# Performance work log

Measured on AMD Instinct MI355X. Metric: run time of the kernel, lower is better.

Reference implementation:

```python
import jax, jax.numpy as jnp
import numpy as np

D_MODEL = 192; D_STATE = 16; EXPAND = 2; D_INNER = EXPAND * D_MODEL
DT_RANK = 12  # ceil(192/16)
SG_HID = 6 * D_STATE  # SimpleGate1D expansion_factor=6
B, H, W = 4, 64, 64

def setup_inputs() -> dict:
    key = jax.random.key(0)
    ks = jax.random.split(key, 24)
    f = lambda i, shape, s=0.02: jax.random.normal(ks[i], shape, jnp.float32) * s
    # dt bias init per SS2D.dt_init: inverse-softplus of dt ~ logU(1e-3, 1e-1)
    dt = jnp.exp(jax.random.uniform(ks[20], (D_INNER,)) * (np.log(0.1) - np.log(0.001)) + np.log(0.001))
    dt = jnp.maximum(dt, 1e-4)
    inv_dt = dt + jnp.log(-jnp.expm1(-dt))
    return {
        "x": jax.random.normal(ks[0], (B, H, W, D_MODEL), jnp.float32),
        "low": jax.random.normal(ks[1], (B, H, W, D_MODEL), jnp.float32),
        "ln_g": jnp.ones((D_MODEL,), jnp.float32), "ln_b": jnp.zeros((D_MODEL,), jnp.float32),
        "in_proj_w": f(2, (2 * D_INNER, D_MODEL)),
        "in_proj_low_w": f(3, (D_INNER, D_MODEL)),
        "conv2d_w": f(4, (D_INNER, 1, 3, 3), 0.1), "conv2d_b": jnp.zeros((D_INNER,), jnp.float32),
        "x_proj_w": f(5, (DT_RANK + 2 * D_STATE, D_INNER)),
        "x_proj_w_low": f(6, (DT_RANK + 2 * D_STATE, D_INNER)),
        "conv_dt_w": f(7, (DT_RANK, 1, 15), 0.05),
        "conv_B_w": f(8, (D_STATE, 1, 15), 0.05),
        "conv_C_w": f(9, (D_STATE, 1, 15), 0.05),
        "sgb_w1": f(10, (2 * SG_HID, D_STATE), 0.1), "sgb_w2": f(11, (D_STATE, SG_HID), 0.1),
        "sgc_w1": f(12, (2 * SG_HID, D_STATE), 0.1), "sgc_w2": f(13, (D_STATE, SG_HID), 0.1),
        "dt_projs_w": f(14, (D_INNER, DT_RANK), 0.2), "dt_projs_b": inv_dt,
        "A_logs": jnp.tile(jnp.log(jnp.arange(1, D_STATE + 1, dtype=jnp.float32))[None, :], (D_INNER, 1)),
        "Ds": jnp.ones((D_INNER,), jnp.float32),
        "out_norm_g": jnp.ones((D_INNER,), jnp.float32), "out_norm_b": jnp.zeros((D_INNER,), jnp.float32),
        "out_proj_w": f(15, (D_MODEL, D_INNER)),
    }

def _ln(x, g, b):
    m = x.mean(-1, keepdims=True)
    v = x.var(-1, keepdims=True)
    return (x - m) * jax.lax.rsqrt(v + 1e-5) * g + b

def _dwconv1d(x, w, dil=2):  # x [B,C,L], w [C,1,K], depthwise, length-preserving
    pad = dil * (w.shape[-1] - 1) // 2
    return jax.lax.conv_general_dilated(x, w, (1,), [(pad, pad)], rhs_dilation=(dil,),
                                        dimension_numbers=('NCH', 'OIH', 'NCH'),
                                        feature_group_count=x.shape[1])

def _sgate(x, w1, w2):  # SimpleGate1D on [B,C,L]: fc1 -> gelu(x1)*x2 -> fc2 along C
    y = jnp.einsum('bcl,hc->bhl', x, w1)
    hid = w2.shape[1]
    g = jax.nn.gelu(y[:, :hid], approximate=False) * y[:, hid:]
    return jnp.einsum('bhl,ch->bcl', g, w2)

def _selective_scan(u, delta, A, Bs, Cs, D):
    # u,delta:[B,Di,L] A:[Di,N] Bs,Cs:[B,N,L] D:[Di]  (Mamba S6 recurrence)
    def step(h, t):
        d_t, u_t, B_t, C_t = t  # [B,Di],[B,Di],[B,N],[B,N]
        h = jnp.exp(d_t[..., None] * A) * h + (d_t * u_t)[..., None] * B_t[:, None, :]
        return h, jnp.einsum('bdn,bn->bd', h, C_t)
    h0 = jnp.zeros((u.shape[0], u.shape[1], A.shape[1]), u.dtype)
    xs = (jnp.moveaxis(delta, -1, 0), jnp.moveaxis(u, -1, 0),
          jnp.moveaxis(Bs, -1, 0), jnp.moveaxis(Cs, -1, 0))
    _, ys = jax.lax.scan(step, h0, xs)  # ys [L,B,Di]
    return jnp.moveaxis(ys, 0, -1) + u * D[:, None]

def reference(x, low, ln_g, ln_b, in_proj_w, in_proj_low_w, conv2d_w, conv2d_b,
              x_proj_w, x_proj_w_low, conv_dt_w, conv_B_w, conv_C_w,
              sgb_w1, sgb_w2, sgc_w1, sgc_w2, dt_projs_w, dt_projs_b,
              A_logs, Ds, out_norm_g, out_norm_b, out_proj_w):
    Bb, Hh, Ww, C = x.shape
    L = Hh * Ww
    R = conv_dt_w.shape[0]
    N = A_logs.shape[1]
    xn = _ln(x, ln_g, ln_b)                       # VSSBlock pre-LN
    xz = xn @ in_proj_w.T                         # [B,H,W,2*Di]
    xh, z = jnp.split(xz, 2, axis=-1)
    lowp = (low @ in_proj_low_w.T).transpose(0, 3, 1, 2)  # [B,Di,H,W]
    xc = xh.transpose(0, 3, 1, 2)
    xc = jax.lax.conv_general_dilated(xc, conv2d_w, (1, 1), [(1, 1), (1, 1)],
                                      dimension_numbers=('NCHW', 'OIHW', 'NCHW'),
                                      feature_group_count=xc.shape[1]) + conv2d_b[None, :, None, None]
    xc = jax.nn.silu(xc)
    xs = xc.reshape(Bb, -1, L)
    lows = lowp.reshape(Bb, -1, L)
    # low-branch projections (dt, B, C) with SimpleGate on B/C
    low_dbl = jnp.einsum('bdl,cd->bcl', lows, x_proj_w_low)
    dts_l, Bs_l, Cs_l = jnp.split(low_dbl, [R, R + N], axis=1)
    Bs_l = _sgate(Bs_l, sgb_w1, sgb_w2)
    Cs_l = _sgate(Cs_l, sgc_w1, sgc_w2)
    # high-branch projections
    x_dbl = jnp.einsum('bdl,cd->bcl', xs, x_proj_w)
    dts, Bs, Cs = jnp.split(x_dbl, [R, R + N], axis=1)
    dts = dts + dts_l; Bs = Bs + Bs_l; Cs = Cs + Cs_l
    # residual dilated depthwise 1D refinement of dt/B/C along L
    dts = dts + _dwconv1d(dts, conv_dt_w)
    Bs = Bs + _dwconv1d(Bs, conv_B_w)
    Cs = Cs + _dwconv1d(Cs, conv_C_w)
    delta = jax.nn.softplus(jnp.einsum('brl,dr->bdl', dts, dt_projs_w) + dt_projs_b[None, :, None])
    y = _selective_scan(xs, delta, -jnp.exp(A_logs), Bs, Cs, Ds)   # [B,Di,L]
    y = _ln(y.reshape(Bb, -1, Hh, Ww).transpose(0, 2, 3, 1), out_norm_g, out_norm_b)
    y = y * jax.nn.silu(z)
    return x + y @ out_proj_w.T  # VSSBlock residual
```

## Files before the change

kernel.cpp:

```cpp
#include <hip/hip_runtime.h>
#include <math.h>

#define LL 4096
#define NBATCH 4
#define CM 192
#define DI 384
#define NST 16
#define RK 12
#define NCH 44
#define SGH 96

typedef unsigned short ushort_t;
typedef __attribute__((ext_vector_type(8))) short bf16x8;
typedef __attribute__((ext_vector_type(4))) float f32x4;
typedef __attribute__((ext_vector_type(8))) unsigned short ushort8;
typedef __attribute__((ext_vector_type(4))) unsigned short ushort4v;

#define O_WT_IN   0
#define O_WT_LOW  147456
#define O_WT_XP   221184
#define O_WT_XPL  245760
#define O_WT_OUT  270336
#define O_XN      344064
#define O_LOWT    3489792
#define O_XH      6635520
#define O_Z       12926976
#define O_LOWP    19218432
#define O_XS      25509888
#define O_DBCH    31801344
#define O_DBCL    32522240
#define O_DBC     33243136
#define O_BS      33964032
#define O_CS      34226176
#define O_DELTA   O_LOWP
#define O_Y       O_XH
#define O_Y1      O_XN
#define O_DTS     O_DBCH

__device__ __forceinline__ ushort_t f2bf(float v) {
    unsigned u = __float_as_uint(v);
    return (ushort_t)((u + 0x7FFFu + ((u >> 16) & 1u)) >> 16);
}
__device__ __forceinline__ float bf2f(ushort_t h) {
    return __uint_as_float(((unsigned)h) << 16);
}

__device__ __forceinline__ int permidx(int l) {
    return ((l >> 2) & 3) * 1024 + ((l >> 4) << 2) + (l & 3);
}

#define LD16P(dst, row, t4) { \
  float4 _a = *(const float4*)((row) + (t4)); \
  float4 _b = *(const float4*)((row) + 1024 + (t4)); \
  float4 _c = *(const float4*)((row) + 2048 + (t4)); \
  float4 _d = *(const float4*)((row) + 3072 + (t4)); \
  dst[0]=_a.x; dst[1]=_a.y; dst[2]=_a.z; dst[3]=_a.w; \
  dst[4]=_b.x; dst[5]=_b.y; dst[6]=_b.z; dst[7]=_b.w; \
  dst[8]=_c.x; dst[9]=_c.y; dst[10]=_c.z; dst[11]=_c.w; \
  dst[12]=_d.x; dst[13]=_d.y; dst[14]=_d.z; dst[15]=_d.w; }

__global__ __launch_bounds__(256) void prep_kernel(
    const float* __restrict__ i0, ushort_t* h0, ushort_t* l0_,
    const float* __restrict__ i1, ushort_t* h1, ushort_t* l1,
    const float* __restrict__ i2, ushort_t* h2, ushort_t* l2,
    const float* __restrict__ p0, ushort_t* ph0, ushort_t* pl0,
    const float* __restrict__ p1, ushort_t* ph1, ushort_t* pl1,
    const float* __restrict__ X, const float* __restrict__ gw, const float* __restrict__ bw,
    ushort_t* __restrict__ oh, ushort_t* __restrict__ ol,
    const float* __restrict__ LOW, ushort_t* __restrict__ lh, ushort_t* __restrict__ llo)
{
    __shared__ float xt[64][193];
    __shared__ float reds[64][4], redq[64][4];
    __shared__ float mu_s[64], rs_s[64];
    int bx = blockIdx.x;
    int tid = threadIdx.x;
    if (bx < 288) {
        const float* in; ushort_t* oh_; ushort_t* ol_; int base;
        if (bx < 144)      { in = i0; oh_ = h0; ol_ = l0_; base = bx * 1024; }
        else if (bx < 216) { in = i1; oh_ = h1; ol_ = l1;  base = (bx-144) * 1024; }
        else               { in = i2; oh_ = h2; ol_ = l2;  base = (bx-216) * 1024; }
        int i = base + tid * 4;
        float4 v = *(const float4*)&in[i];
        ushort4v h, l;
        h.x = f2bf(v.x); l.x = f2bf(v.x - bf2f(h.x));
        h.y = f2bf(v.y); l.y = f2bf(v.y - bf2f(h.y));
        h.z = f2bf(v.z); l.z = f2bf(v.z - bf2f(h.z));
        h.w = f2bf(v.w); l.w = f2bf(v.w - bf2f(h.w));
        *(ushort4v*)&oh_[i] = h;
        *(ushort4v*)&ol_[i] = l;
        return;
    }
    if (bx < 336) {
        int bb = bx - 288;
        int sel = bb / 24, bxx = bb % 24;
        const float* in = sel ? p1 : p0;
        ushort_t* oh_ = sel ? ph1 : ph0;
        ushort_t* ol_ = sel ? pl1 : pl0;
        int idx = (bxx * 256 + tid) * 4;
        int n = idx / 384;
        float4 v = (n < NCH) ? *(const float4*)&in[idx] : make_float4(0.f,0.f,0.f,0.f);
        ushort4v h, l;
        h.x = f2bf(v.x); l.x = f2bf(v.x - bf2f(h.x));
        h.y = f2bf(v.y); l.y = f2bf(v.y - bf2f(h.y));
        h.z = f2bf(v.z); l.z = f2bf(v.z - bf2f(h.z));
        h.w = f2bf(v.w); l.w = f2bf(v.w - bf2f(h.w));
        *(ushort4v*)&oh_[idx] = h;
        *(ushort4v*)&ol_[idx] = l;
        return;
    }
    int ax = bx - 336;
    if (ax >= 256) {
        int i = ((ax - 256) * 256 + tid) * 4;
        float4 v = *(const float4*)&LOW[i];
        ushort4v h, l;
        h.x = f2bf(v.x); l.x = f2bf(v.x - bf2f(h.x));
        h.y = f2bf(v.y); l.y = f2bf(v.y - bf2f(h.y));
        h.z = f2bf(v.z); l.z = f2bf(v.z - bf2f(h.z));
        h.w = f2bf(v.w); l.w = f2bf(v.w - bf2f(h.w));
        *(ushort4v*)&lh[i] = h;
        *(ushort4v*)&llo[i] = l;
        return;
    }
    int t0 = ax * 64;
    const float* Xb = X + (size_t)t0 * CM;
#pragma unroll
    for (int i = 0; i < 12; i++) {
        int f4 = tid + 256 * i;
        float4 v = *(const float4*)&Xb[f4 * 4];
        int row = f4 / 48, c = (f4 % 48) * 4;
        xt[row][c] = v.x; xt[row][c+1] = v.y; xt[row][c+2] = v.z; xt[row][c+3] = v.w;
    }
    __syncthreads();
    int tok = tid & 63, p = tid >> 6;
    float s = 0.f, q = 0.f;
#pragma unroll 8
    for (int i = 0; i < 48; i++) { float v = xt[tok][p*48+i]; s += v; q = fmaf(v, v, q); }
    reds[tok][p] = s; redq[tok][p] = q;
    __syncthreads();
    if (tid < 64) {
        float ss = reds[tid][0]+reds[tid][1]+reds[tid][2]+reds[tid][3];
        float qq = redq[tid][0]+redq[tid][1]+redq[tid][2]+redq[tid][3];
        float mu = ss * (1.f/CM);
        float var = qq * (1.f/CM) - mu*mu;
        mu_s[tid] = mu; rs_s[tid] = rsqrtf(var + 1e-5f);
    }
    __syncthreads();
    int tok2 = tid >> 2, c0 = (tid & 3) * 48;
    float mu = mu_s[tok2], rs = rs_s[tok2];
    size_t tb = (size_t)(t0 + tok2) * CM;
#pragma unroll 8
    for (int i = 0; i < 48; i++) {
        int c = c0 + i;
        float v = (xt[tok2][c] - mu) * rs * gw[c] + bw[c];
        ushort_t h = f2bf(v);
        oh[tb + c] = h;
        ol[tb + c] = f2bf(v - bf2f(h));
    }
}

__global__ __launch_bounds__(256) void gemm_inlow(
    const ushort_t* __restrict__ xnh, const ushort_t* __restrict__ xnl,
    const ushort_t* __restrict__ wInH, const ushort_t* __restrict__ wInL,
    const ushort_t* __restrict__ lowh, const ushort_t* __restrict__ lowl,
    const ushort_t* __restrict__ wLowH, const ushort_t* __restrict__ wLowL,
    float* __restrict__ xh, float* __restrict__ z, float* __restrict__ lowp)
{
    __shared__ __align__(16) char smem[32768];
    ushort_t* sAh = (ushort_t*)smem;
    ushort_t* sAl = sAh + 4096;
    ushort_t* sWh = sAh + 8192;
    ushort_t* sWl = sAh + 12288;
    const int KDIM = 192;
    int tid = threadIdx.x;
    int t0 = blockIdx.x * 128;
    int b = t0 >> 12, l0 = t0 & 4095;
    int ysel = blockIdx.y;
    bool isLow = ysel >= 6;
    int n0 = (isLow ? (ysel - 6) : ysel) * 128;
    const ushort_t* Ahi = isLow ? lowh : xnh;
    const ushort_t* Alo = isLow ? lowl : xnl;
    const ushort_t* Whi = isLow ? wLowH : wInH;
    const ushort_t* Wlo = isLow ? wLowL : wInL;
    int arow = tid >> 1, kgA = (tid & 1) * 2;
    const ushort_t* gAh = Ahi + (size_t)(t0 + arow) * KDIM + kgA * 8;
    const ushort_t* gAl = Alo + (size_t)(t0 + arow) * KDIM + kgA * 8;
    const ushort_t* gWh = Whi + (size_t)(n0 + arow) * KDIM + kgA * 8;
    const ushort_t* gWl = Wlo + (size_t)(n0 + arow) * KDIM + kgA * 8;
    int lane = tid & 63, w = tid >> 6;
    int ln = lane & 15, kg = lane >> 4;
    int am0 = w * 32 + ln;
    f32x4 acc[2][8];
#pragma unroll
    for (int mf = 0; mf < 2; mf++)
#pragma unroll
        for (int nf = 0; nf < 8; nf++) acc[mf][nf] = (f32x4){0.f, 0.f, 0.f, 0.f};

    for (int k0 = 0; k0 < KDIM; k0 += 32) {
        __syncthreads();
        {
            ushort8 a0 = *(const ushort8*)(gAh + k0);
            ushort8 a1 = *(const ushort8*)(gAh + k0 + 8);
            *(ushort8*)(sAh + kgA*1024 + arow*8) = a0;
            *(ushort8*)(sAh + (kgA+1)*1024 + arow*8) = a1;
            ushort8 b0 = *(const ushort8*)(gAl + k0);
            ushort8 b1 = *(const ushort8*)(gAl + k0 + 8);
            *(ushort8*)(sAl + kgA*1024 + arow*8) = b0;
            *(ushort8*)(sAl + (kgA+1)*1024 + arow*8) = b1;
            ushort8 w0 = *(const ushort8*)(gWh + k0);
            ushort8 w1 = *(const ushort8*)(gWh + k0 + 8);
            *(ushort8*)(sWh + kgA*1024 + arow*8) = w0;
            *(ushort8*)(sWh + (kgA+1)*1024 + arow*8) = w1;
            ushort8 w2 = *(const ushort8*)(gWl + k0);
            ushort8 w3 = *(const ushort8*)(gWl + k0 + 8);
            *(ushort8*)(sWl + kgA*1024 + arow*8) = w2;
            *(ushort8*)(sWl + (kgA+1)*1024 + arow*8) = w3;
        }
        __syncthreads();
        bf16x8 aH[2], aL[2];
#pragma unroll
        for (int mf = 0; mf < 2; mf++) {
            aH[mf] = *(const bf16x8*)(sAh + kg*1024 + (am0 + mf*16)*8);
            aL[mf] = *(const bf16x8*)(sAl + kg*1024 + (am0 + mf*16)*8);
        }
#pragma unroll
        for (int half = 0; half < 2; half++) {
            bf16x8 bH[4], bL[4];
#pragma unroll
            for (int n4 = 0; n4 < 4; n4++) {
                int nr = (half*4 + n4)*16 + ln;
                bH[n4] = *(const bf16x8*)(sWh + kg*1024 + nr*8);
                bL[n4] = *(const bf16x8*)(sWl + kg*1024 + nr*8);
            }
#pragma unroll
            for (int mf = 0; mf < 2; mf++)
#pragma unroll
                for (int n4 = 0; n4 < 4; n4++) {
                    int nf = half*4 + n4;
                    acc[mf][nf] = __builtin_amdgcn_mfma_f32_16x16x32_bf16(aH[mf], bH[n4], acc[mf][nf], 0, 0, 0);
                    acc[mf][nf] = __builtin_amdgcn_mfma_f32_16x16x32_bf16(aH[mf], bL[n4], acc[mf][nf], 0, 0, 0);
                    acc[mf][nf] = __builtin_amdgcn_mfma_f32_16x16x32_bf16(aL[mf], bH[n4], acc[mf][nf], 0, 0, 0);
                }
        }
    }
#pragma unroll
    for (int mf = 0; mf < 2; mf++) {
        int l = l0 + w*32 + mf*16 + kg*4;
#pragma unroll
        for (int nf = 0; nf < 8; nf++) {
            int n = n0 + nf*16 + ln;
            float* dst;
            if (!isLow) {
                dst = (n < DI) ? (xh + ((size_t)b*DI + n)*LL + l)
                               : (z  + ((size_t)b*DI + (n - DI))*LL + l);
            } else {
                dst = lowp + ((size_t)b*DI + n)*LL + l;
            }
            *(f32x4*)dst = acc[mf][nf];
        }
    }
}

template<int MODE, int SPLIT, int PERM0>
__global__ __launch_bounds__(256) void gemm_cmaj(
    const float* __restrict__ A0, const float* __restrict__ A1,
    const ushort_t* __restrict__ W0h, const ushort_t* __restrict__ W0l,
    const ushort_t* __restrict__ W1h, const ushort_t* __restrict__ W1l,
    const float* __restrict__ resid,
    float* __restrict__ o0, float* __restrict__ o1, int Nreal)
{
    __shared__ __align__(16) float sA[32*68];
    __shared__ __align__(16) ushort_t sWh[4*64*8];
    __shared__ __align__(16) ushort_t sWl[4*64*8];
    bool sel = (blockIdx.z == 1);
    const float* A = sel ? A1 : A0;
    const ushort_t* Wh = sel ? W1h : W0h;
    const ushort_t* Wl = sel ? W1l : W0l;
    float* out0 = sel ? o1 : o0;
    const bool perm = sel ? false : (PERM0 != 0);
    int tid = threadIdx.x;
    int t0 = blockIdx.x * 64;
    int b = t0 >> 12, l0 = t0 & 4095;
    int n0 = blockIdx.y * 64;
    const float* Ab = A + (size_t)b * 384 * LL;
    int wrow = tid >> 2, kgW = tid & 3;
    int lane = tid & 63, w = tid >> 6;
    int ln = lane & 15, kg = lane >> 4;
    int am0 = w * 16 + ln;
    f32x4 acc[4];
#pragma unroll
    for (int nf = 0; nf < 4; nf++) acc[nf] = (f32x4){0.f, 0.f, 0.f, 0.f};

    for (int k0 = 0; k0 < 384; k0 += 32) {
        __syncthreads();
#pragma unroll
        for (int i = 0; i < 2; i++) {
            int idx = tid + 256*i;
            int row = idx >> 4, ch = idx & 15;
            int m = ch * 4;
            int src = perm ? (((m >> 2) & 3) * 1024 + (((l0 + m) >> 4) << 2))
                           : (l0 + m);
            float4 v = *(const float4*)&Ab[(size_t)(k0 + row)*LL + src];
            *(float4*)&sA[row*68 + m] = v;
        }
        {
            ushort8 wv = *(const ushort8*)(Wh + (size_t)(n0 + wrow)*384 + k0 + kgW*8);
            *(ushort8*)(sWh + kgW*512 + wrow*8) = wv;
            if (SPLIT == 3) {
                ushort8 wl = *(const ushort8*)(Wl + (size_t)(n0 + wrow)*384 + k0 + kgW*8);
                *(ushort8*)(sWl + kgW*512 + wrow*8) = wl;
            }
        }
        __syncthreads();
        bf16x8 aH, aL;
#pragma unroll
        for (int e = 0; e < 8; e++) {
            float v = sA[(kg*8 + e)*68 + am0];
            ushort_t h = f2bf(v);
            aH[e] = (short)h;
            if (SPLIT == 3) aL[e] = (short)f2bf(v - bf2f(h));
        }
        bf16x8 bH[4], bL[4];
#pragma unroll
        for (int nf = 0; nf < 4; nf++) {
            bH[nf] = *(const bf16x8*)(sWh + kg*512 + (nf*16 + ln)*8);
            if (SPLIT == 3) bL[nf] = *(const bf16x8*)(sWl + kg*512 + (nf*16 + ln)*8);
        }
#pragma unroll
        for (int nf = 0; nf < 4; nf++) {
            acc[nf] = __builtin_amdgcn_mfma_f32_16x16x32_bf16(aH, bH[nf], acc[nf], 0, 0, 0);
            if (SPLIT == 3) {
                acc[nf] = __builtin_amdgcn_mfma_f32_16x16x32_bf16(aH, bL[nf], acc[nf], 0, 0, 0);
                acc[nf] = __builtin_amdgcn_mfma_f32_16x16x32_bf16(aL, bH[nf], acc[nf], 0, 0, 0);
            }
        }
    }

    if (MODE == 2) {
#pragma unroll
        for (int j = 0; j < 4; j++) {
            int t = t0 + w*16 + kg*4 + j;
#pragma unroll
            for (int nf = 0; nf < 4; nf++) {
                int n = n0 + nf*16 + ln;
                out0[(size_t)t*CM + n] = resid[(size_t)t*CM + n] + acc[nf][j];
            }
        }
    } else {
        int l = l0 + w*16 + kg*4;
#pragma unroll
        for (int nf = 0; nf < 4; nf++) {
            int n = n0 + nf*16 + ln;
            if (n < Nreal)
                *(f32x4*)(out0 + ((size_t)b*Nreal + n)*LL + l) = acc[nf];
        }
    }
}

__global__ __launch_bounds__(256) void conv2d_silu_kernel(const float* __restrict__ xh,
    const float* __restrict__ w, const float* __restrict__ bias, float* __restrict__ xs)
{
    int tid = threadIdx.x;
    int l = blockIdx.x * 256 + tid;
    int c = blockIdx.y, b = blockIdx.z;
    const float* P = xh + ((size_t)b*DI + c)*LL;
    int h = l >> 6, ww = l & 63;
    float acc = bias[c];
#pragma unroll
    for (int kh = 0; kh < 3; kh++) {
        int hh = h + kh - 1;
        if ((unsigned)hh < 64u) {
#pragma unroll
            for (int kw = 0; kw < 3; kw++) {
                int wv = ww + kw - 1;
                if ((unsigned)wv < 64u) acc = fmaf(w[c*9 + kh*3 + kw], P[hh*64 + wv], acc);
            }
        }
    }
    float sg = 1.f / (1.f + __expf(-acc));
    xs[((size_t)b*DI + c)*LL + permidx(l)] = acc * sg;
}

__global__ __launch_bounds__(256) void gates_kernel(const float* __restrict__ dbcH,
    const float* __restrict__ dbcL,
    const float* __restrict__ sgb1, const float* __restrict__ sgb2,
    const float* __restrict__ sgc1, const float* __restrict__ sgc2,
    float* __restrict__ dbc)
{
    __shared__ float w1[192*16];
    __shared__ float w2[16*96];
    __shared__ float red[4][16][64];
    int tid = threadIdx.x;
    int gate = blockIdx.z;
    const float* g1 = gate ? sgc1 : sgb1;
    const float* g2 = gate ? sgc2 : sgb2;
    for (int i = tid; i < 192*16; i += 256) w1[i] = g1[i];
    for (int i = tid; i < 16*96;  i += 256) w2[i] = g2[i];
    int lq = tid & 63, p = tid >> 6;
    int l = blockIdx.x * 64 + lq;
    int b = blockIdx.y;
    size_t pb_ = (size_t)b*NCH*LL + l;
    __syncthreads();
    if (!gate) {
#pragma unroll
        for (int i = 0; i < 3; i++) {
            int c = p*3 + i;
            dbc[pb_ + (size_t)c*LL] = dbcH[pb_ + (size_t)c*LL] + dbcL[pb_ + (size_t)c*LL];
        }
    }
    int coff = RK + gate*NST;
    float xin[16], og[16];
#pragma unroll
    for (int n = 0; n < 16; n++) { xin[n] = dbcL[pb_ + (size_t)(coff+n)*LL]; og[n] = 0.f; }
    int h0 = p * 24;
    for (int h = h0; h < h0 + 24; h++) {
        float ya = 0.f, yb = 0.f;
#pragma unroll
        for (int n = 0; n < 16; n++) {
            ya = fmaf(w1[h*16+n], xin[n], ya);
            yb = fmaf(w1[(h+SGH)*16+n], xin[n], yb);
        }
        float gg = 0.5f * ya * (1.f + erff(ya * 0.70710678f)) * yb;
#pragma unroll
        for (int n = 0; n < 16; n++) og[n] = fmaf(w2[n*SGH+h], gg, og[n]);
    }
#pragma unroll
    for (int n = 0; n < 16; n++) red[p][n][lq] = og[n];
    __syncthreads();
#pragma unroll
    for (int i = 0; i < 4; i++) {
        int n = p*4 + i;
        float v = red[0][n][lq] + red[1][n][lq] + red[2][n][lq] + red[3][n][lq];
        dbc[pb_ + (size_t)(coff+n)*LL] = dbcH[pb_ + (size_t)(coff+n)*LL] + v;
    }
}

__global__ __launch_bounds__(256) void conv_dbc_kernel(const float* __restrict__ dbc,
    const float* __restrict__ wdt, const float* __restrict__ wB, const float* __restrict__ wC,
    float* __restrict__ dts, float* __restrict__ Bs, float* __restrict__ Cs)
{
    int l = blockIdx.x * 256 + threadIdx.x;
    int c = blockIdx.y, b = blockIdx.z;
    const float* wsrc = (c < RK) ? (wdt + c*15)
                      : (c < RK+NST ? wB + (c-RK)*15 : wC + (c-RK-NST)*15);
    float w[15];
#pragma unroll
    for (int k = 0; k < 15; k++) w[k] = wsrc[k];
    const float* P = dbc + ((size_t)b*NCH + c)*LL;
    float a = P[l];
#pragma unroll
    for (int k = 0; k < 15; k++) {
        int lt = l + 2*k - 14;
        if ((unsigned)lt < (unsigned)LL) a = fmaf(w[k], P[lt], a);
    }
    if (c < RK)            dts[((size_t)b*RK  + c)*LL + l] = a;
    else if (c < RK+NST)   Bs [((size_t)b*NST + (c-RK))*LL + permidx(l)] = a;
    else                   Cs [((size_t)b*NST + (c-RK-NST))*LL + permidx(l)] = a;
}

__global__ __launch_bounds__(256) void delta_kernel(const float* __restrict__ dts,
    const float* __restrict__ dtw, const float* __restrict__ dtb, float* __restrict__ delta)
{
    __shared__ float sdt[RK][128];
    __shared__ float sw[64][RK];
    int tid = threadIdx.x;
    int l0 = blockIdx.x * 128, d0 = blockIdx.y * 64, b = blockIdx.z;
    for (int i = tid; i < RK*128; i += 256) {
        int r = i >> 7, lq = i & 127;
        sdt[r][lq] = dts[((size_t)b*RK + r)*LL + l0 + lq];
    }
    for (int i = tid; i < 64*RK; i += 256) {
        int dq = i / RK, r = i - dq*RK;
        sw[dq][r] = dtw[(size_t)(d0+dq)*RK + r];
    }
    __syncthreads();
    int lq = tid & 63, g = tid >> 6;
    for (int dd = 0; dd < 16; dd++) {
        int dqq = g*16 + dd, d = d0 + dqq;
        float wr[RK];
#pragma unroll
        for (int r = 0; r < RK; r++) wr[r] = sw[dqq][r];
        float bias = dtb[d];
#pragma unroll
        for (int li = 0; li < 2; li++) {
            int lloc = lq + li*64;
            float s = bias;
#pragma unroll
            for (int r = 0; r < RK; r++) s = fmaf(wr[r], sdt[r][lloc], s);
            float sp = fmaxf(s, 0.f) + __logf(1.f + __expf(-fabsf(s)));
            delta[((size_t)b*DI + d)*LL + permidx(l0 + lloc)] = sp;
        }
    }
}

__global__ __launch_bounds__(256) void scan_kernel(
    const float* __restrict__ u_, const float* __restrict__ delta_,
    const float* __restrict__ Bs_, const float* __restrict__ Cs_,
    const float* __restrict__ Alogs, const float* __restrict__ Ds,
    float* __restrict__ y0_, float* __restrict__ y1_)
{
    __shared__ float wAs[8][4], wBs[8][4];
    __shared__ float yt[16][258];
    int tid = threadIdx.x;
    int t4 = tid * 4;
    int bid = blockIdx.x;
    int half = bid & 1, bd = bid >> 1;
    int b = bd / DI, d = bd % DI;
    int n0 = half * 8;
    size_t rowoff = ((size_t)b*DI + d)*LL;
    float dl[16], du[16], yac[16];
    LD16P(du, u_ + rowoff, t4);
    LD16P(dl, delta_ + rowoff, t4);
    float Dd = Ds[d];
#pragma unroll
    for (int s = 0; s < 16; s++) {
        yac[s] = half ? 0.f : du[s]*Dd;
        du[s] = dl[s]*du[s];
    }
    int lane = tid & 63, w = tid >> 6;
#pragma unroll 1
    for (int j = 0; j < 8; j++) {
        float An = -__expf(Alogs[d*NST + n0 + j]);
        float Bn[16], Cn[16], t[16];
        LD16P(Bn, Bs_ + ((size_t)b*NST + n0 + j)*LL, t4);
        LD16P(Cn, Cs_ + ((size_t)b*NST + n0 + j)*LL, t4);
        float a = 1.f, h = 0.f;
#pragma unroll
        for (int s = 0; s < 16; s++) {
            float e = __expf(dl[s]*An);
            a *= e;
            h = fmaf(e, h, du[s]*Bn[s]);
            yac[s] = fmaf(Cn[s], h, yac[s]);
            t[s] = Cn[s]*a;
        }
        float ap = a, hv = h;
        for (int off = 1; off < 64; off <<= 1) {
            float pa = __shfl_up(ap, (unsigned)off, 64);
            float pb = __shfl_up(hv, (unsigned)off, 64);
            if (lane >= off) { hv = fmaf(ap, pb, hv); ap *= pa; }
        }
        if (lane == 63) { wAs[j][w] = ap; wBs[j][w] = hv; }
        __syncthreads();
        float PB = 0.f;
        for (int ww = 0; ww < w; ww++) PB = fmaf(wAs[j][ww], PB, wBs[j][ww]);
        hv = fmaf(ap, PB, hv);
        float tt = __shfl_up(hv, 1u, 64);
        float hin = lane ? tt : PB;
#pragma unroll
        for (int s = 0; s < 16; s++) yac[s] = fmaf(t[s], hin, yac[s]);
    }
#pragma unroll
    for (int i = 0; i < 16; i++) yt[i][tid] = yac[i];
    __syncthreads();
    float* yout = (half ? y1_ : y0_) + rowoff;
#pragma unroll
    for (int r = 0; r < 16; r++)
        yout[r*256 + tid] = yt[tid & 15][r*16 + (tid >> 4)];
}

__global__ __launch_bounds__(1024) void outnorm_gate_kernel(const float* __restrict__ y0,
    float* y1g, const float* __restrict__ z,
    const float* __restrict__ g, const float* __restrict__ bt)
{
    __shared__ float rs_[16][64], rq_[16][64];
    __shared__ float mu_s[64], rstd_s[64];
    int tid = threadIdx.x;
    int lq = tid & 63, p = tid >> 6;
    int l = blockIdx.x * 64 + lq;
    int b = blockIdx.y;
    const float* yp0 = y0 + (size_t)b*DI*LL + l;
    float* yp1 = y1g + (size_t)b*DI*LL + l;
    float s = 0.f, q = 0.f;
#pragma unroll 4
    for (int i = 0; i < 24; i++) {
        int d = p*24 + i;
        float v = yp0[(size_t)d*LL] + yp1[(size_t)d*LL];
        s += v; q = fmaf(v, v, q);
    }
    rs_[p][lq] = s; rq_[p][lq] = q;
    __syncthreads();
    if (p == 0) {
        float ss = 0.f, qq = 0.f;
#pragma unroll
        for (int i = 0; i < 16; i++) { ss += rs_[i][lq]; qq += rq_[i][lq]; }
        float mu = ss * (1.f/DI);
        float var = qq * (1.f/DI) - mu*mu;
        mu_s[lq] = mu; rstd_s[lq] = rsqrtf(var + 1e-5f);
    }
    __syncthreads();
    float mu = mu_s[lq], rs = rstd_s[lq];
    const float* zp = z + (size_t)b*DI*LL + l;
#pragma unroll 4
    for (int i = 0; i < 24; i++) {
        int d = p*24 + i;
        float v = ((yp0[(size_t)d*LL] + yp1[(size_t)d*LL]) - mu)*rs*g[d] + bt[d];
        float zv = zp[(size_t)d*LL];
        float sg = 1.f / (1.f + __expf(-zv));
        yp1[(size_t)d*LL] = v * (zv * sg);
    }
}

extern "C" void kernel_launch(void* const* d_in, const int* in_sizes, int n_in,
                              void* d_out, int out_size, void* d_ws, size_t ws_size,
                              hipStream_t stream)
{
    (void)in_sizes; (void)n_in; (void)out_size; (void)ws_size;
    const float* x     = (const float*)d_in[0];
    const float* low   = (const float*)d_in[1];
    const float* ln_g  = (const float*)d_in[2];
    const float* ln_b  = (const float*)d_in[3];
    const float* w_in  = (const float*)d_in[4];
    const float* w_low = (const float*)d_in[5];
    const float* w_c2d = (const float*)d_in[6];
    const float* b_c2d = (const float*)d_in[7];
    const float* w_xp  = (const float*)d_in[8];
    const float* w_xpl = (const float*)d_in[9];
    const float* w_cdt = (const float*)d_in[10];
    const float* w_cB  = (const float*)d_in[11];
    const float* w_cC  = (const float*)d_in[12];
    const float* sgb1  = (const float*)d_in[13];
    const float* sgb2  = (const float*)d_in[14];
    const float* sgc1  = (const float*)d_in[15];
    const float* sgc2  = (const float*)d_in[16];
    const float* dtw   = (const float*)d_in[17];
    const float* dtb   = (const float*)d_in[18];
    const float* Alogs = (const float*)d_in[19];
    const float* Ds    = (const float*)d_in[20];
    const float* ong   = (const float*)d_in[21];
    const float* onb   = (const float*)d_in[22];
    const float* w_out = (const float*)d_in[23];
    float* ws  = (float*)d_ws;
    float* out = (float*)d_out;
    dim3 blk(256);

    ushort_t* wInH  = (ushort_t*)(ws + O_WT_IN);   ushort_t* wInL  = wInH + 147456;
    ushort_t* wLowH = (ushort_t*)(ws + O_WT_LOW);  ushort_t* wLowL = wLowH + 73728;
    ushort_t* wOutH = (ushort_t*)(ws + O_WT_OUT);  ushort_t* wOutL = wOutH + 73728;
    ushort_t* wXpH  = (ushort_t*)(ws + O_WT_XP);   ushort_t* wXpL  = wXpH + 24576;
    ushort_t* wXplH = (ushort_t*)(ws + O_WT_XPL);  ushort_t* wXplL = wXplH + 24576;
    ushort_t* xnh   = (ushort_t*)(ws + O_XN);      ushort_t* xnl   = xnh + 3145728;
    ushort_t* lowh  = (ushort_t*)(ws + O_LOWT);    ushort_t* lowl  = lowh + 3145728;

    prep_kernel<<<3664, blk, 0, stream>>>(w_in, wInH, wInL, w_low, wLowH, wLowL,
                                          w_out, wOutH, wOutL,
                                          w_xp, wXpH, wXpL, w_xpl, wXplH, wXplL,
                                          x, ln_g, ln_b, xnh, xnl, low, lowh, lowl);

    gemm_inlow<<<dim3(128,9), blk, 0, stream>>>(xnh, xnl, wInH, wInL,
                                                lowh, lowl, wLowH, wLowL,
                                                ws+O_XH, ws+O_Z, ws+O_LOWP);

    conv2d_silu_kernel<<<dim3(16,384,4), blk, 0, stream>>>(ws+O_XH, w_c2d, b_c2d, ws+O_XS);

    gemm_cmaj<1,3,1><<<dim3(256,1,2), blk, 0, stream>>>(ws+O_XS, ws+O_LOWP,
                                                        wXpH, wXpL, wXplH, wXplL,
                                                        nullptr, ws+O_DBCH, ws+O_DBCL, NCH);

    gates_kernel<<<dim3(64,4,2), blk, 0, stream>>>(ws+O_DBCH, ws+O_DBCL, sgb1, sgb2, sgc1, sgc2, ws+O_DBC);

    conv_dbc_kernel<<<dim3(16,44,4), blk, 0, stream>>>(ws+O_DBC, w_cdt, w_cB, w_cC,
                                                       ws+O_DTS, ws+O_BS, ws+O_CS);
    delta_kernel<<<dim3(32,6,4), blk, 0, stream>>>(ws+O_DTS, dtw, dtb, ws+O_DELTA);

    scan_kernel<<<3072, blk, 0, stream>>>(ws+O_XS, ws+O_DELTA, ws+O_BS, ws+O_CS, Alogs, Ds,
                                          ws+O_Y, ws+O_Y1);

    outnorm_gate_kernel<<<dim3(64,4), dim3(1024), 0, stream>>>(ws+O_Y, ws+O_Y1, ws+O_Z, ong, onb);

    gemm_cmaj<2,1,0><<<dim3(256,3,1), blk, 0, stream>>>(ws+O_Y1, nullptr,
                                                        wOutH, wOutL, nullptr, nullptr,
                                                        x, out, nullptr, CM);
}
```

Measured before the change: 235.1 us.

## Store xh and z as bf16, vectorize conv2d, specialize scan for A=-(n+1)

The input-projection GEMM now writes the xh and z intermediates as bf16 instead of fp32, halving their write and read traffic in conv2d and the out-norm gate. The depthwise conv2d kernel handles four tokens per thread with hoisted weights and a vectorized permuted store. The scan kernel checks at runtime whether A equals -(n+1) and, if so, replaces the per-step exp with repeated multiplication by exp(-delta). That path avoids most transcendental calls but compounds rounding error, and the bf16 intermediates lower precision.

```diff
diff --git a/kernel.cpp b/kernel.cpp
--- a/kernel.cpp
+++ b/kernel.cpp
@@ -163,7 +163,7 @@
     const ushort_t* __restrict__ wInH, const ushort_t* __restrict__ wInL,
     const ushort_t* __restrict__ lowh, const ushort_t* __restrict__ lowl,
     const ushort_t* __restrict__ wLowH, const ushort_t* __restrict__ wLowL,
-    float* __restrict__ xh, float* __restrict__ z, float* __restrict__ lowp)
+    ushort_t* __restrict__ xhb, ushort_t* __restrict__ zb, float* __restrict__ lowp)
 {
     __shared__ __align__(16) char smem[32768];
     ushort_t* sAh = (ushort_t*)smem;
@@ -248,14 +248,16 @@
 #pragma unroll
         for (int nf = 0; nf < 8; nf++) {
             int n = n0 + nf*16 + ln;
-            float* dst;
             if (!isLow) {
-                dst = (n < DI) ? (xh + ((size_t)b*DI + n)*LL + l)
-                               : (z  + ((size_t)b*DI + (n - DI))*LL + l);
+                ushort4v hv;
+#pragma unroll
+                for (int j = 0; j < 4; j++) hv[j] = f2bf(acc[mf][nf][j]);
+                ushort_t* dstb = (n < DI) ? (xhb + ((size_t)b*DI + n)*LL + l)
+                                          : (zb  + ((size_t)b*DI + (n - DI))*LL + l);
+                *(ushort4v*)dstb = hv;
             } else {
-                dst = lowp + ((size_t)b*DI + n)*LL + l;
-            }
-            *(f32x4*)dst = acc[mf][nf];
+                *(f32x4*)(lowp + ((size_t)b*DI + n)*LL + l) = acc[mf][nf];
+            }
         }
     }
 }
@@ -356,28 +358,43 @@
     }
 }
 
-__global__ __launch_bounds__(256) void conv2d_silu_kernel(const float* __restrict__ xh,
+__global__ __launch_bounds__(256) void conv2d_silu_kernel(const ushort_t* __restrict__ xhb,
     const float* __restrict__ w, const float* __restrict__ bias, float* __restrict__ xs)
 {
     int tid = threadIdx.x;
-    int l = blockIdx.x * 256 + tid;
+    int l0 = (blockIdx.x * 256 + tid) * 4;
     int c = blockIdx.y, b = blockIdx.z;
-    const float* P = xh + ((size_t)b*DI + c)*LL;
-    int h = l >> 6, ww = l & 63;
-    float acc = bias[c];
+    const ushort_t* P = xhb + ((size_t)b*DI + c)*LL;
+    int h = l0 >> 6, w0 = l0 & 63;
+    float wc[9];
+#pragma unroll
+    for (int k = 0; k < 9; k++) wc[k] = w[c*9 + k];
+    float bs = bias[c];
+    float av[4] = {bs, bs, bs, bs};
 #pragma unroll
     for (int kh = 0; kh < 3; kh++) {
         int hh = h + kh - 1;
         if ((unsigned)hh < 64u) {
-#pragma unroll
-            for (int kw = 0; kw < 3; kw++) {
-                int wv = ww + kw - 1;
-                if ((unsigned)wv < 64u) acc = fmaf(w[c*9 + kh*3 + kw], P[hh*64 + wv], acc);
-            }
-        }
-    }
-    float sg = 1.f / (1.f + __expf(-acc));
-    xs[((size_t)b*DI + c)*LL + permidx(l)] = acc * sg;
+            const ushort_t* R = P + hh*64;
+#pragma unroll
+            for (int j = 0; j < 4; j++) {
+#pragma unroll
+                for (int kw = 0; kw < 3; kw++) {
+                    int wv = w0 + j + kw - 1;
+                    if ((unsigned)wv < 64u)
+                        av[j] = fmaf(wc[kh*3 + kw], bf2f(R[wv]), av[j]);
+                }
+            }
+        }
+    }
+    f32x4 o;
+#pragma unroll
+    for (int j = 0; j < 4; j++) {
+        float sg = 1.f / (1.f + __expf(-av[j]));
+        o[j] = av[j] * sg;
+    }
+    int pb = ((l0 >> 2) & 3) * 1024 + ((l0 >> 4) << 2);
+    *(f32x4*)&xs[((size_t)b*DI + c)*LL + pb] = o;
 }
 
 __global__ __launch_bounds__(256) void gates_kernel(const float* __restrict__ dbcH,
@@ -516,37 +533,91 @@
         yac[s] = half ? 0.f : du[s]*Dd;
         du[s] = dl[s]*du[s];
     }
+    bool fast = true;
+#pragma unroll 1
+    for (int n = 0; n < 8; n++) {
+        float An = -__expf(Alogs[d*NST + n0 + n]);
+        float tgt = (float)(n0 + n + 1);
+        fast = fast && (fabsf(An + tgt) < 1e-3f * tgt);
+    }
     int lane = tid & 63, w = tid >> 6;
+    if (fast) {
+        float E[16];
+#pragma unroll
+        for (int s = 0; s < 16; s++) dl[s] = __expf(-dl[s]);
+        if (half) {
+#pragma unroll
+            for (int s = 0; s < 16; s++) {
+                float t2 = dl[s]*dl[s];
+                float t4v = t2*t2;
+                E[s] = t4v*t4v;
+            }
+        } else {
+#pragma unroll
+            for (int s = 0; s < 16; s++) E[s] = 1.f;
+        }
 #pragma unroll 1
-    for (int j = 0; j < 8; j++) {
-        float An = -__expf(Alogs[d*NST + n0 + j]);
-        float Bn[16], Cn[16], t[16];
-        LD16P(Bn, Bs_ + ((size_t)b*NST + n0 + j)*LL, t4);
-        LD16P(Cn, Cs_ + ((size_t)b*NST + n0 + j)*LL, t4);
-        float a = 1.f, h = 0.f;
-#pragma unroll
-        for (int s = 0; s < 16; s++) {
-            float e = __expf(dl[s]*An);
-            a *= e;
-            h = fmaf(e, h, du[s]*Bn[s]);
-            yac[s] = fmaf(Cn[s], h, yac[s]);
-            t[s] = Cn[s]*a;
-        }
-        float ap = a, hv = h;
-        for (int off = 1; off < 64; off <<= 1) {
-            float pa = __shfl_up(ap, (unsigned)off, 64);
-            float pb = __shfl_up(hv, (unsigned)off, 64);
-            if (lane >= off) { hv = fmaf(ap, pb, hv); ap *= pa; }
-        }
-        if (lane == 63) { wAs[j][w] = ap; wBs[j][w] = hv; }
-        __syncthreads();
-        float PB = 0.f;
-        for (int ww = 0; ww < w; ww++) PB = fmaf(wAs[j][ww], PB, wBs[j][ww]);
-        hv = fmaf(ap, PB, hv);
-        float tt = __shfl_up(hv, 1u, 64);
-        float hin = lane ? tt : PB;
-#pragma unroll
-        for (int s = 0; s < 16; s++) yac[s] = fmaf(t[s], hin, yac[s]);
+        for (int j = 0; j < 8; j++) {
+            float Bn[16], Cn[16], t[16];
+            LD16P(Bn, Bs_ + ((size_t)b*NST + n0 + j)*LL, t4);
+            LD16P(Cn, Cs_ + ((size_t)b*NST + n0 + j)*LL, t4);
+            float a = 1.f, h = 0.f;
+#pragma unroll
+            for (int s = 0; s < 16; s++) {
+                E[s] *= dl[s];
+                a *= E[s];
+                h = fmaf(E[s], h, du[s]*Bn[s]);
+                yac[s] = fmaf(Cn[s], h, yac[s]);
+                t[s] = Cn[s]*a;
+            }
+            float ap = a, hv = h;
+            for (int off = 1; off < 64; off <<= 1) {
+                float pa = __shfl_up(ap, (unsigned)off, 64);
+                float pb = __shfl_up(hv, (unsigned)off, 64);
+                if (lane >= off) { hv = fmaf(ap, pb, hv); ap *= pa; }
+            }
+            if (lane == 63) { wAs[j][w] = ap; wBs[j][w] = hv; }
+            __syncthreads();
+            float PB = 0.f;
+            for (int ww = 0; ww < w; ww++) PB = fmaf(wAs[j][ww], PB, wBs[j][ww]);
+            hv = fmaf(ap, PB, hv);
+            float tt = __shfl_up(hv, 1u, 64);
+            float hin = lane ? tt : PB;
+#pragma unroll
+            for (int s = 0; s < 16; s++) yac[s] = fmaf(t[s], hin, yac[s]);
+        }
+    } else {
+#pragma unroll 1
+        for (int j = 0; j < 8; j++) {
+            float An = -__expf(Alogs[d*NST + n0 + j]);
+            float Bn[16], Cn[16], t[16];
+            LD16P(Bn, Bs_ + ((size_t)b*NST + n0 + j)*LL, t4);
+            LD16P(Cn, Cs_ + ((size_t)b*NST + n0 + j)*LL, t4);
+            float a = 1.f, h = 0.f;
+#pragma unroll
+            for (int s = 0; s < 16; s++) {
+                float e = __expf(dl[s]*An);
+                a *= e;
+                h = fmaf(e, h, du[s]*Bn[s]);
+                yac[s] = fmaf(Cn[s], h, yac[s]);
+                t[s] = Cn[s]*a;
+            }
+            float ap = a, hv = h;
+            for (int off = 1; off < 64; off <<= 1) {
+                float pa = __shfl_up(ap, (unsigned)off, 64);
+                float pb = __shfl_up(hv, (unsigned)off, 64);
+                if (lane >= off) { hv = fmaf(ap, pb, hv); ap *= pa; }
+            }
+            if (lane == 63) { wAs[j][w] = ap; wBs[j][w] = hv; }
+            __syncthreads();
+            float PB = 0.f;
+            for (int ww = 0; ww < w; ww++) PB = fmaf(wAs[j][ww], PB, wBs[j][ww]);
+            hv = fmaf(ap, PB, hv);
+            float tt = __shfl_up(hv, 1u, 64);
+            float hin = lane ? tt : PB;
+#pragma unroll
+            for (int s = 0; s < 16; s++) yac[s] = fmaf(t[s], hin, yac[s]);
+        }
     }
 #pragma unroll
     for (int i = 0; i < 16; i++) yt[i][tid] = yac[i];
@@ -558,7 +629,7 @@
 }
 
 __global__ __launch_bounds__(1024) void outnorm_gate_kernel(const float* __restrict__ y0,
-    float* y1g, const float* __restrict__ z,
+    float* y1g, const ushort_t* __restrict__ zb,
     const float* __restrict__ g, const float* __restrict__ bt)
 {
     __shared__ float rs_[16][64], rq_[16][64];
@@ -588,12 +659,12 @@
     }
     __syncthreads();
     float mu = mu_s[lq], rs = rstd_s[lq];
-    const float* zp = z + (size_t)b*DI*LL + l;
+    const ushort_t* zp = zb + (size_t)b*DI*LL + l;
 #pragma unroll 4
     for (int i = 0; i < 24; i++) {
         int d = p*24 + i;
         float v = ((yp0[(size_t)d*LL] + yp1[(size_t)d*LL]) - mu)*rs*g[d] + bt[d];
-        float zv = zp[(size_t)d*LL];
+        float zv = bf2f(zp[(size_t)d*LL]);
         float sg = 1.f / (1.f + __expf(-zv));
         yp1[(size_t)d*LL] = v * (zv * sg);
     }
@@ -639,6 +710,8 @@
     ushort_t* wXplH = (ushort_t*)(ws + O_WT_XPL);  ushort_t* wXplL = wXplH + 24576;
     ushort_t* xnh   = (ushort_t*)(ws + O_XN);      ushort_t* xnl   = xnh + 3145728;
     ushort_t* lowh  = (ushort_t*)(ws + O_LOWT);    ushort_t* lowl  = lowh + 3145728;
+    ushort_t* xhb   = (ushort_t*)(ws + O_XH);
+    ushort_t* zb    = (ushort_t*)(ws + O_Z);
 
     prep_kernel<<<3664, blk, 0, stream>>>(w_in, wInH, wInL, w_low, wLowH, wLowL,
                                           w_out, wOutH, wOutL,
@@ -647,9 +720,9 @@
 
     gemm_inlow<<<dim3(128,9), blk, 0, stream>>>(xnh, xnl, wInH, wInL,
                                                 lowh, lowl, wLowH, wLowL,
-                                                ws+O_XH, ws+O_Z, ws+O_LOWP);
-
-    conv2d_silu_kernel<<<dim3(16,384,4), blk, 0, stream>>>(ws+O_XH, w_c2d, b_c2d, ws+O_XS);
+                                                xhb, zb, ws+O_LOWP);
+
+    conv2d_silu_kernel<<<dim3(4,384,4), blk, 0, stream>>>(xhb, w_c2d, b_c2d, ws+O_XS);
 
     gemm_cmaj<1,3,1><<<dim3(256,1,2), blk, 0, stream>>>(ws+O_XS, ws+O_LOWP,
                                                         wXpH, wXpL, wXplH, wXplL,
@@ -664,7 +737,7 @@
     scan_kernel<<<3072, blk, 0, stream>>>(ws+O_XS, ws+O_DELTA, ws+O_BS, ws+O_CS, Alogs, Ds,
                                           ws+O_Y, ws+O_Y1);
 
-    outnorm_gate_kernel<<<dim3(64,4), dim3(1024), 0, stream>>>(ws+O_Y, ws+O_Y1, ws+O_Z, ong, onb);
+    outnorm_gate_kernel<<<dim3(64,4), dim3(1024), 0, stream>>>(ws+O_Y, ws+O_Y1, zb, ong, onb);
 
     gemm_cmaj<2,1,0><<<dim3(256,3,1), blk, 0, stream>>>(ws+O_Y1, nullptr,
                                                         wOutH, wOutL, nullptr, nullptr,
```

Result: faster. 211.5 us (-10.0%).
